# Kernel tuning notes

Measured on AMD Instinct MI355X. Metric: run time of the kernel, lower is better.

The kernel has to match this reference:

```python
import jax, jax.numpy as jnp
import numpy as np

N = 8192      # num_nodes
D_IN = 561    # input feature dim (HAR)
D_H = 256     # hidden / encoder dim
E = 262144    # edges per view (~32 avg degree)
NCLS = 6
LAMBDA = 1.0


def _gat_att(row, col, H, v0, v1, n):
    # per-edge sigmoid logits + row-wise segment softmax (sparse_softmax)
    f1 = (H @ v0)[:, 0]                      # (N,)
    f2 = (H @ v1)[:, 0]
    u = jax.nn.sigmoid(f1[row] + f2[col])    # (E,)
    rmax = jax.ops.segment_max(u, row, num_segments=n)
    ex = jnp.exp(u - rmax[row])
    rsum = jax.ops.segment_sum(ex, row, num_segments=n)
    return ex / (rsum[row] + 1e-12)


def _spmm(row, col, vals, H, n):
    # sparse.mm(C, H): out[row] += vals * H[col]
    return jax.ops.segment_sum(vals[:, None] * H[col], row, num_segments=n)


def setup_inputs() -> dict:
    key = jax.random.key(0)
    ks = jax.random.split(key, 30)

    def xav(k, shp):
        lim = np.sqrt(6.0 / (shp[0] + shp[1]))
        return jax.random.uniform(k, shp, jnp.float32, -lim, lim)

    inp = {}
    inp["X"] = jax.random.normal(ks[0], (N, D_IN), jnp.float32)
    inp["X2"] = jax.random.normal(ks[1], (N, D_IN), jnp.float32)
    inp["Theta"] = jax.random.normal(ks[2], (N, N), jnp.float32)
    inp["A_idx"] = jax.random.randint(ks[3], (2, E), 0, N)
    inp["A_vals"] = jax.random.uniform(ks[4], (E,), jnp.float32)
    inp["A2_idx"] = jax.random.randint(ks[5], (2, E), 0, N)
    inp["A2_vals"] = jax.random.uniform(ks[6], (E,), jnp.float32)
    inp["S"] = jax.random.randint(ks[7], (E,), 0, N)
    inp["R"] = jax.random.randint(ks[8], (E,), 0, N)
    inp["S2"] = jax.random.randint(ks[9], (E,), 0, N)
    inp["R2"] = jax.random.randint(ks[10], (E,), 0, N)
    inp["p"] = jax.random.randint(ks[11], (N,), 0, NCLS)
    inp["Labels"] = jax.random.randint(ks[12], (N,), 0, NCLS)
    # parameters (single encoder layer, shared across views as in the source)
    inp["W0"] = xav(ks[13], (D_IN, D_H))
    inp["v00"] = xav(ks[14], (D_H, 1))
    inp["v10"] = xav(ks[15], (D_H, 1))
    inp["weight"] = jnp.full((N, N), 1e-4, jnp.float32)
    inp["fc1_w"] = xav(ks[16], (512, D_H))
    inp["fc1_b"] = jnp.zeros((512,), jnp.float32)
    inp["fcz_w"] = xav(ks[17], (NCLS, 512))
    inp["fcz_b"] = jnp.zeros((NCLS,), jnp.float32)
    inp["fc2_w"] = xav(ks[18], (512, D_H))
    inp["fc2_b"] = jnp.zeros((512,), jnp.float32)
    inp["fcz2_w"] = xav(ks[19], (NCLS, 512))
    inp["fcz2_b"] = jnp.zeros((NCLS,), jnp.float32)
    return inp


def reference(X, X2, Theta, A_idx, A_vals, A2_idx, A2_vals, S, R, S2, R2, p, Labels,
              W0, v00, v10, weight, fc1_w, fc1_b, fcz_w, fcz_b,
              fc2_w, fc2_b, fcz2_w, fcz2_b):
    n = weight.shape[0]
    coef = weight - jnp.diag(jnp.diagonal(weight))   # zero the diagonal
    rowA, colA = A_idx[0], A_idx[1]
    rowB, colB = A2_idx[0], A2_idx[1]

    # ---- view 1: encode -> self-expression -> decode ----
    H = X @ W0                                        # (N, D_H)
    att1 = _gat_att(rowA, colA, H, v00, v10, n)       # (E,)
    H_enc1 = _spmm(rowA, colA, att1, H, n)            # (N, D_H)
    HC = coef @ H_enc1                                # (N, D_H)
    X_recon = _spmm(rowA, colA, att1, HC @ W0.T, n)   # (N, D_IN)
    z = (H_enc1 @ fc1_w.T + fc1_b) @ fcz_w.T + fcz_b  # (N, 6)

    # ---- view 2 (shares W0/v00/v10 as in the source) ----
    H2 = X2 @ W0
    att2 = _gat_att(rowB, colB, H2, v00, v10, n)
    H_enc2 = _spmm(rowB, colB, att2, H2, n)
    HC2 = coef @ H_enc2
    X2_recon = _spmm(rowB, colB, att2, HC2 @ W0.T, n)
    z2 = (H_enc2 @ fc2_w.T + fc2_b) @ fcz2_w.T + fcz2_b

    # ---- losses ----
    features_loss = ((X - X_recon) ** 2).sum() + ((X2 - X2_recon) ** 2).sum()
    SE_loss = 0.5 * ((H_enc1 - HC) ** 2).sum() + 0.5 * ((H_enc2 - HC2) ** 2).sum()
    S_Regular = jnp.abs(coef).sum()
    Cq_loss = jnp.abs(coef.T * Theta).sum()

    def ce_sum(logits):
        lp = jax.nn.log_softmax(logits, axis=-1)
        return -jnp.take_along_axis(lp, p[:, None], axis=1).sum()

    dense_loss = ce_sum(z) + ce_sum(z2)

    structure_loss = (-jax.nn.log_sigmoid((H_enc1[S] * H_enc1[R]).sum(-1)).sum()
                      - jax.nn.log_sigmoid((H_enc2[S2] * H_enc2[R2]).sum(-1)).sum())
    consistent_loss = ((H_enc1 - H_enc2) ** 2).sum()

    pre_loss = (features_loss + LAMBDA * structure_loss + 10.0 * SE_loss
                + 0.01 * consistent_loss + 1.0 * S_Regular)
    loss = (0.01 * features_loss + LAMBDA * structure_loss + 10.0 * SE_loss
            + 0.001 * consistent_loss + 1.0 * S_Regular + 5.0 * Cq_loss
            + 5.0 * dense_loss)
    return (pre_loss, loss, dense_loss, features_loss, structure_loss, SE_loss,
            coef, consistent_loss, S_Regular, Cq_loss, H_enc1, H_enc2)
```

## Files before the change

kernel.cpp:

```cpp
#include <hip/hip_runtime.h>
#include <math.h>

#define NNODES 8192
#define DIN 561
#define DH 256
#define NEDGE 262144
#define FCDIM 512
#define MLD 576

enum { AC_FEAT = 0, AC_STRUCT, AC_SE, AC_CONS, AC_SREG, AC_CQ, AC_DENSE, AC_NUM };
#define NBUCKET 64

#define OFF_COEF ((size_t)6)
#define OFF_CONS ((size_t)6 + (size_t)NNODES * NNODES)
#define OFF_SREG (OFF_CONS + 1)
#define OFF_CQ   (OFF_CONS + 2)
#define OFF_H1   (OFF_CONS + 3)
#define OFF_H2   (OFF_H1 + (size_t)NNODES * DH)

typedef short bf16x8 __attribute__((ext_vector_type(8)));
typedef float f32x4  __attribute__((ext_vector_type(4)));

__device__ __forceinline__ unsigned short f2bf(float f) {
    union { float f; unsigned int u; } v; v.f = f;
    const unsigned int u = v.u;
    return (unsigned short)((u + 0x7fffu + ((u >> 16) & 1u)) >> 16);
}

__device__ __forceinline__ void gload_lds16(const void* g, void* l) {
    __builtin_amdgcn_global_load_lds(
        (const __attribute__((address_space(1))) unsigned int*)g,
        (__attribute__((address_space(3))) unsigned int*)l, 16, 0, 0);
}

__global__ __launch_bounds__(256) void gate_gemm_nn(
    const float* __restrict__ A, const float* __restrict__ B,
    float* __restrict__ C, int M, int Nn, int K, int lda, int ldb, int ldc)
{
    __shared__ float As[32][68];
    __shared__ float Bs[32][68];
    const int bm = blockIdx.x * 64, bn = blockIdx.y * 64;
    const int tid = threadIdx.x;
    const int tx = tid & 15, ty = tid >> 4;
    float acc[4][4] = {};
    for (int k0 = 0; k0 < K; k0 += 32) {
        const int ar = tid >> 2, ak = (tid & 3) * 8;
        #pragma unroll
        for (int j = 0; j < 8; ++j) {
            const int gk = k0 + ak + j;
            As[ak + j][ar] = (gk < K) ? A[(size_t)(bm + ar) * lda + gk] : 0.f;
        }
        const int bk = tid >> 3, bn0 = (tid & 7) * 8;
        const int gk = k0 + bk;
        #pragma unroll
        for (int j = 0; j < 8; ++j) {
            const int gn = bn + bn0 + j;
            Bs[bk][bn0 + j] = (gk < K && gn < Nn) ? B[(size_t)gk * ldb + gn] : 0.f;
        }
        __syncthreads();
        #pragma unroll
        for (int k = 0; k < 32; ++k) {
            float a[4], b[4];
            #pragma unroll
            for (int i = 0; i < 4; ++i) a[i] = As[k][ty * 4 + i];
            #pragma unroll
            for (int j = 0; j < 4; ++j) b[j] = Bs[k][tx * 4 + j];
            #pragma unroll
            for (int i = 0; i < 4; ++i)
                #pragma unroll
                for (int j = 0; j < 4; ++j) acc[i][j] = fmaf(a[i], b[j], acc[i][j]);
        }
        __syncthreads();
    }
    #pragma unroll
    for (int i = 0; i < 4; ++i) {
        const int gm = bm + ty * 4 + i;
        if (gm >= M) continue;
        #pragma unroll
        for (int j = 0; j < 4; ++j) {
            const int gn = bn + tx * 4 + j;
            if (gn < Nn) C[(size_t)gm * ldc + gn] = acc[i][j];
        }
    }
}

__global__ __launch_bounds__(256) void gate_gemm_bt(
    const float* __restrict__ A, int lda,
    const float* __restrict__ B,
    const float* __restrict__ bias,
    float* __restrict__ C, int ldc, int M, int Nn, int K)
{
    __shared__ float As[32][68];
    __shared__ float Bs[32][68];
    const int bm = blockIdx.x * 64, bn = blockIdx.y * 64;
    const int tid = threadIdx.x;
    const int tx = tid & 15, ty = tid >> 4;
    float acc[4][4] = {};
    for (int k0 = 0; k0 < K; k0 += 32) {
        const int ar = tid >> 2, ak = (tid & 3) * 8;
        #pragma unroll
        for (int j = 0; j < 8; ++j)
            As[ak + j][ar] = A[(size_t)(bm + ar) * lda + k0 + ak + j];
        const int br = tid >> 2, bk = (tid & 3) * 8;
        const int gn = bn + br;
        #pragma unroll
        for (int j = 0; j < 8; ++j)
            Bs[bk + j][br] = (gn < Nn) ? B[(size_t)gn * K + k0 + bk + j] : 0.f;
        __syncthreads();
        #pragma unroll
        for (int k = 0; k < 32; ++k) {
            float a[4], b[4];
            #pragma unroll
            for (int i = 0; i < 4; ++i) a[i] = As[k][ty * 4 + i];
            #pragma unroll
            for (int j = 0; j < 4; ++j) b[j] = Bs[k][tx * 4 + j];
            #pragma unroll
            for (int i = 0; i < 4; ++i)
                #pragma unroll
                for (int j = 0; j < 4; ++j) acc[i][j] = fmaf(a[i], b[j], acc[i][j]);
        }
        __syncthreads();
    }
    #pragma unroll
    for (int i = 0; i < 4; ++i) {
        const int gm = bm + ty * 4 + i;
        if (gm >= M) continue;
        #pragma unroll
        for (int j = 0; j < 4; ++j) {
            const int gn = bn + tx * 4 + j;
            if (gn < Nn) {
                float v = acc[i][j];
                if (bias) v += bias[gn];
                C[(size_t)gm * ldc + gn] = v;
            }
        }
    }
}

__global__ __launch_bounds__(256) void gate_gemm_coef(
    const float* __restrict__ W, const float* __restrict__ B, float* __restrict__ C)
{
    __shared__ float As[16][132];
    __shared__ float Bs[16][64];
    const int bm = blockIdx.x * 128, bn = blockIdx.y * 64;
    const int tid = threadIdx.x;
    const int tx = tid & 15, ty = tid >> 4;
    float acc[8][4] = {};
    for (int k0 = 0; k0 < NNODES; k0 += 16) {
        const int ar = tid >> 1, ak = (tid & 1) * 8;
        const float* Ap = W + (size_t)(bm + ar) * NNODES + k0 + ak;
        const bool maskdiag = (k0 + 15 >= bm) && (k0 <= bm + 127);
        if (maskdiag) {
            #pragma unroll
            for (int j = 0; j < 8; ++j) {
                float v = Ap[j];
                if (bm + ar == k0 + ak + j) v = 0.f;
                As[ak + j][ar] = v;
            }
        } else {
            const float4 v0 = *(const float4*)(Ap);
            const float4 v1 = *(const float4*)(Ap + 4);
            As[ak + 0][ar] = v0.x; As[ak + 1][ar] = v0.y;
            As[ak + 2][ar] = v0.z; As[ak + 3][ar] = v0.w;
            As[ak + 4][ar] = v1.x; As[ak + 5][ar] = v1.y;
            As[ak + 6][ar] = v1.z; As[ak + 7][ar] = v1.w;
        }
        const int bk = tid >> 4, bn0 = (tid & 15) * 4;
        *(float4*)&Bs[bk][bn0] = *(const float4*)(B + (size_t)(k0 + bk) * 512 + bn + bn0);
        __syncthreads();
        #pragma unroll
        for (int k = 0; k < 16; ++k) {
            float a[8], b[4];
            #pragma unroll
            for (int i = 0; i < 8; ++i) a[i] = As[k][ty * 8 + i];
            #pragma unroll
            for (int j = 0; j < 4; ++j) b[j] = Bs[k][tx * 4 + j];
            #pragma unroll
            for (int i = 0; i < 8; ++i)
                #pragma unroll
                for (int j = 0; j < 4; ++j) acc[i][j] = fmaf(a[i], b[j], acc[i][j]);
        }
        __syncthreads();
    }
    #pragma unroll
    for (int i = 0; i < 8; ++i) {
        float4 v = make_float4(acc[i][0], acc[i][1], acc[i][2], acc[i][3]);
        *(float4*)(C + (size_t)(bm + ty * 8 + i) * 512 + bn + tx * 4) = v;
    }
}

#define BMT 128
#define BNT 64
#define BKT 64

__global__ __launch_bounds__(256, 2) void gate_gemm_coef_mfma(
    const unsigned short* __restrict__ Wbf,
    const unsigned short* __restrict__ Bt,
    float* __restrict__ C)
{
    __shared__ __align__(16) unsigned short Asm[2][BMT * BKT];
    __shared__ __align__(16) unsigned short Bsm[2][BNT * BKT];
    const int tid = threadIdx.x;
    const int wid = tid >> 6, lane = tid & 63;
    const int bm = blockIdx.x * BMT, bn = blockIdx.y * BNT;
    const int wr = wid >> 1, wc = wid & 1;

    const int l3 = lane >> 3, l7 = lane & 7;
    const int kxor = (l7 ^ l3) * 8;
    const unsigned short* aSrc[4];
    int aDst[4];
    #pragma unroll
    for (int i = 0; i < 4; ++i) {
        const int c = wid + i * 4;
        const int r = c * 8 + l3;
        aSrc[i] = Wbf + (size_t)(bm + r) * NNODES + kxor;
        aDst[i] = c * 512;
    }
    const unsigned short* bSrc[2];
    int bDst[2];
    #pragma unroll
    for (int i = 0; i < 2; ++i) {
        const int c = wid + i * 4;
        const int r = c * 8 + l3;
        bSrc[i] = Bt + (size_t)(bn + r) * NNODES + kxor;
        bDst[i] = c * 512;
    }

    const int l15 = lane & 15, l4 = lane >> 4;
    int aOff[2][4], bOff[2][2];
    #pragma unroll
    for (int ks = 0; ks < 2; ++ks) {
        const int u = ks * 4 + l4;
        #pragma unroll
        for (int mr = 0; mr < 4; ++mr) {
            const int r = wr * 64 + mr * 16 + l15;
            aOff[ks][mr] = r * 64 + ((u ^ (r & 7)) * 8);
        }
        #pragma unroll
        for (int nr = 0; nr < 2; ++nr) {
            const int r = wc * 32 + nr * 16 + l15;
            bOff[ks][nr] = r * 64 + ((u ^ (r & 7)) * 8);
        }
    }

    f32x4 acc[4][2];
    #pragma unroll
    for (int i = 0; i < 4; ++i)
        #pragma unroll
        for (int j = 0; j < 2; ++j) acc[i][j] = (f32x4){0.f, 0.f, 0.f, 0.f};

    #pragma unroll
    for (int i = 0; i < 4; ++i) { gload_lds16(aSrc[i], &Asm[0][aDst[i]]); aSrc[i] += BKT; }
    #pragma unroll
    for (int i = 0; i < 2; ++i) { gload_lds16(bSrc[i], &Bsm[0][bDst[i]]); bSrc[i] += BKT; }
    __syncthreads();

    int cur = 0;
    const int NT = NNODES / BKT;
    for (int t = 0; t < NT; ++t) {
        if (t + 1 < NT) {
            const int nxt = cur ^ 1;
            #pragma unroll
            for (int i = 0; i < 4; ++i) { gload_lds16(aSrc[i], &Asm[nxt][aDst[i]]); aSrc[i] += BKT; }
            #pragma unroll
            for (int i = 0; i < 2; ++i) { gload_lds16(bSrc[i], &Bsm[nxt][bDst[i]]); bSrc[i] += BKT; }
        }
        const unsigned short* Ab = &Asm[cur][0];
        const unsigned short* Bb = &Bsm[cur][0];
        #pragma unroll
        for (int ks = 0; ks < 2; ++ks) {
            bf16x8 av[4], bv[2];
            #pragma unroll
            for (int mr = 0; mr < 4; ++mr) av[mr] = *(const bf16x8*)(Ab + aOff[ks][mr]);
            #pragma unroll
            for (int nr = 0; nr < 2; ++nr) bv[nr] = *(const bf16x8*)(Bb + bOff[ks][nr]);
            #pragma unroll
            for (int mr = 0; mr < 4; ++mr)
                #pragma unroll
                for (int nr = 0; nr < 2; ++nr)
                    acc[mr][nr] = __builtin_amdgcn_mfma_f32_16x16x32_bf16(
                        av[mr], bv[nr], acc[mr][nr], 0, 0, 0);
        }
        __syncthreads();
        cur ^= 1;
    }

    #pragma unroll
    for (int mr = 0; mr < 4; ++mr) {
        const int grow0 = bm + wr * 64 + mr * 16 + l4 * 4;
        #pragma unroll
        for (int nr = 0; nr < 2; ++nr) {
            const int gcol = bn + wc * 32 + nr * 16 + l15;
            float* cp = C + (size_t)grow0 * 512 + gcol;
            #pragma unroll
            for (int q = 0; q < 4; ++q) cp[(size_t)q * 512] = acc[mr][nr][q];
        }
    }
}

__global__ __launch_bounds__(256) void gate_hcat_bt(
    const float* __restrict__ Hcat, unsigned short* __restrict__ Bt)
{
    __shared__ float Ts[64][65];
    const int i0 = blockIdx.x * 64;
    const int j0 = blockIdx.y * 64;
    const int c = threadIdx.x & 63, g = threadIdx.x >> 6;
    #pragma unroll
    for (int ii = 0; ii < 16; ++ii) {
        const int r = g * 16 + ii;
        Ts[r][c] = Hcat[(size_t)(i0 + r) * 512 + j0 + c];
    }
    __syncthreads();
    #pragma unroll
    for (int ii = 0; ii < 16; ++ii) {
        const int r = g * 16 + ii;
        Bt[(size_t)(j0 + r) * NNODES + i0 + c] = f2bf(Ts[c][r]);
    }
}

__global__ __launch_bounds__(256) void gate_f1f2(
    const float* __restrict__ H, const float* __restrict__ v0,
    const float* __restrict__ v1, float* __restrict__ f1, float* __restrict__ f2)
{
    const int wave = threadIdx.x >> 6, lane = threadIdx.x & 63;
    const int row = blockIdx.x * 4 + wave;
    const float4 h = ((const float4*)(H + (size_t)row * DH))[lane];
    const float4 a = ((const float4*)v0)[lane];
    const float4 b = ((const float4*)v1)[lane];
    float s1 = h.x * a.x + h.y * a.y + h.z * a.z + h.w * a.w;
    float s2 = h.x * b.x + h.y * b.y + h.z * b.z + h.w * b.w;
    #pragma unroll
    for (int off = 32; off; off >>= 1) {
        s1 += __shfl_down(s1, off);
        s2 += __shfl_down(s2, off);
    }
    if (lane == 0) { f1[row] = s1; f2[row] = s2; }
}

__global__ void gate_hist(const int* __restrict__ rows, int* __restrict__ cnt)
{
    const int e = blockIdx.x * 256 + threadIdx.x;
    if (e < NEDGE) atomicAdd(&cnt[rows[e]], 1);
}

__global__ __launch_bounds__(256) void gate_scan(
    const int* __restrict__ cnt, int* __restrict__ rowptr, int* __restrict__ cur)
{
    __shared__ int part[256];
    const int t = threadIdx.x;
    const int base = t * 32;
    int local[32];
    int s = 0;
    #pragma unroll
    for (int i = 0; i < 32; ++i) { local[i] = s; s += cnt[base + i]; }
    part[t] = s;
    __syncthreads();
    for (int d = 1; d < 256; d <<= 1) {
        const int add = (t >= d) ? part[t - d] : 0;
        __syncthreads();
        part[t] += add;
        __syncthreads();
    }
    const int excl = (t == 0) ? 0 : part[t - 1];
    #pragma unroll
    for (int i = 0; i < 32; ++i) {
        const int v = excl + local[i];
        rowptr[base + i] = v;
        cur[base + i] = v;
    }
    if (t == 255) rowptr[NNODES] = excl + s;
}

__global__ void gate_scatter(const int* __restrict__ rows, const int* __restrict__ cols,
                             int* __restrict__ cur, int* __restrict__ col_p)
{
    const int e = blockIdx.x * 256 + threadIdx.x;
    if (e < NEDGE) {
        const int slot = atomicAdd(&cur[rows[e]], 1);
        col_p[slot] = cols[e];
    }
}

__global__ __launch_bounds__(64) void gate_att(
    const int* __restrict__ rowptr, const int* __restrict__ col_p,
    const float* __restrict__ f1, const float* __restrict__ f2,
    float* __restrict__ att_p)
{
    const int row = blockIdx.x;
    const int s0 = rowptr[row], s1 = rowptr[row + 1];
    const int lane = threadIdx.x;
    const float f1r = f1[row];
    float mx = -1e30f;
    for (int s = s0 + lane; s < s1; s += 64) {
        float u = f1r + f2[col_p[s]];
        u = 1.f / (1.f + expf(-u));
        att_p[s] = u;
        mx = fmaxf(mx, u);
    }
    #pragma unroll
    for (int off = 32; off; off >>= 1) mx = fmaxf(mx, __shfl_xor(mx, off));
    float sum = 0.f;
    for (int s = s0 + lane; s < s1; s += 64) {
        const float ex = expf(att_p[s] - mx);
        att_p[s] = ex;
        sum += ex;
    }
    #pragma unroll
    for (int off = 32; off; off >>= 1) sum += __shfl_xor(sum, off);
    const float inv = 1.f / (sum + 1e-12f);
    for (int s = s0 + lane; s < s1; s += 64) att_p[s] *= inv;
}

__global__ __launch_bounds__(256) void gate_spmm_henc(
    const int* __restrict__ rowptr, const int* __restrict__ col_p,
    const float* __restrict__ att_p, const float* __restrict__ H,
    float* __restrict__ Hcat, float* __restrict__ outp, int voff)
{
    const int row = blockIdx.x, d = threadIdx.x;
    const int s0 = rowptr[row], s1 = rowptr[row + 1];
    float acc = 0.f;
    for (int s = s0; s < s1; ++s)
        acc = fmaf(att_p[s], H[(size_t)col_p[s] * DH + d], acc);
    Hcat[(size_t)row * 512 + voff + d] = acc;
    outp[(size_t)row * DH + d] = acc;
}

__global__ __launch_bounds__(256) void gate_coef(
    const float* __restrict__ W, const float* __restrict__ Theta,
    float* __restrict__ coef_out, double* __restrict__ accumB,
    unsigned short* __restrict__ wbf)
{
    __shared__ float Ts[64][65];
    __shared__ float red[256];
    const int i0 = blockIdx.x * 64, j0 = blockIdx.y * 64;
    const int t = threadIdx.x;
    const int c = t & 63, rgrp = t >> 6;
    #pragma unroll
    for (int jj = 0; jj < 16; ++jj) {
        const int jr = rgrp * 16 + jj;
        Ts[jr][c] = Theta[(size_t)(j0 + jr) * NNODES + i0 + c];
    }
    __syncthreads();
    float sreg = 0.f, cq = 0.f;
    #pragma unroll
    for (int ii = 0; ii < 16; ++ii) {
        const int rr = rgrp * 16 + ii;
        const int gi = i0 + rr, gj = j0 + c;
        const float w = W[(size_t)gi * NNODES + gj];
        const float cf = (gi == gj) ? 0.f : w;
        coef_out[(size_t)gi * NNODES + gj] = cf;
        if (wbf) wbf[(size_t)gi * NNODES + gj] = f2bf(cf);
        const float a = fabsf(cf);
        sreg += a;
        cq = fmaf(a, fabsf(Ts[c][rr]), cq);
    }
    const int bucket = (blockIdx.x + blockIdx.y) & (NBUCKET - 1);
    red[t] = sreg; __syncthreads();
    for (int d = 128; d; d >>= 1) { if (t < d) red[t] += red[t + d]; __syncthreads(); }
    if (t == 0) atomicAdd(&accumB[bucket * AC_NUM + AC_SREG], (double)red[0]);
    __syncthreads();
    red[t] = cq; __syncthreads();
    for (int d = 128; d; d >>= 1) { if (t < d) red[t] += red[t + d]; __syncthreads(); }
    if (t == 0) atomicAdd(&accumB[bucket * AC_NUM + AC_CQ], (double)red[0]);
}

__global__ __launch_bounds__(256) void gate_se(
    const float* __restrict__ Hcat, const float* __restrict__ HC,
    double* __restrict__ accumB)
{
    __shared__ float red[256];
    float part = 0.f;
    for (size_t i = (size_t)blockIdx.x * 256 + threadIdx.x;
         i < (size_t)NNODES * 512; i += (size_t)2048 * 256) {
        const float d = Hcat[i] - HC[i];
        part = fmaf(d, d, part);
    }
    const int t = threadIdx.x;
    red[t] = part; __syncthreads();
    for (int d = 128; d; d >>= 1) { if (t < d) red[t] += red[t + d]; __syncthreads(); }
    if (t == 0) atomicAdd(&accumB[(blockIdx.x & (NBUCKET - 1)) * AC_NUM + AC_SE], (double)red[0]);
}

__global__ __launch_bounds__(256) void gate_cons(
    const float* __restrict__ Hcat, double* __restrict__ accumB)
{
    __shared__ float red[256];
    float part = 0.f;
    for (size_t i = (size_t)blockIdx.x * 256 + threadIdx.x;
         i < (size_t)NNODES * DH; i += (size_t)1024 * 256) {
        const size_t row = i >> 8;
        const int d = (int)(i & 255);
        const float v = Hcat[row * 512 + d] - Hcat[row * 512 + 256 + d];
        part = fmaf(v, v, part);
    }
    const int t = threadIdx.x;
    red[t] = part; __syncthreads();
    for (int d = 128; d; d >>= 1) { if (t < d) red[t] += red[t + d]; __syncthreads(); }
    if (t == 0) atomicAdd(&accumB[(blockIdx.x & (NBUCKET - 1)) * AC_NUM + AC_CONS], (double)red[0]);
}

__global__ __launch_bounds__(256) void gate_recon_loss(
    const int* __restrict__ rowptr, const int* __restrict__ col_p,
    const float* __restrict__ att_p, const float* __restrict__ Mbuf,
    const float* __restrict__ X, double* __restrict__ accumB)
{
    __shared__ float red[256];
    const int row = blockIdx.x, t = threadIdx.x;
    const int s0 = rowptr[row], s1 = rowptr[row + 1];
    float acc0 = 0.f, acc1 = 0.f, acc2 = 0.f;
    for (int s = s0; s < s1; ++s) {
        const float a = att_p[s];
        const float* mr = Mbuf + (size_t)col_p[s] * MLD;
        acc0 = fmaf(a, mr[t], acc0);
        acc1 = fmaf(a, mr[t + 256], acc1);
        if (t < DIN - 512) acc2 = fmaf(a, mr[t + 512], acc2);
    }
    const float* xr = X + (size_t)row * DIN;
    const float d0 = xr[t] - acc0;
    const float d1 = xr[t + 256] - acc1;
    float part = d0 * d0 + d1 * d1;
    if (t < DIN - 512) { const float d2 = xr[t + 512] - acc2; part = fmaf(d2, d2, part); }
    red[t] = part; __syncthreads();
    for (int d = 128; d; d >>= 1) { if (t < d) red[t] += red[t + d]; __syncthreads(); }
    if (t == 0) atomicAdd(&accumB[(blockIdx.x & (NBUCKET - 1)) * AC_NUM + AC_FEAT], (double)red[0]);
}

__global__ __launch_bounds__(256) void gate_struct(
    const int* __restrict__ S, const int* __restrict__ R,
    const float* __restrict__ Hcat, int voff, double* __restrict__ accumB)
{
    __shared__ float red[4];
    const int wave = threadIdx.x >> 6, lane = threadIdx.x & 63;
    const int widx = blockIdx.x * 4 + wave;
    float part = 0.f;
    for (int e = widx; e < NEDGE; e += gridDim.x * 4) {
        const float4 av = ((const float4*)(Hcat + (size_t)S[e] * 512 + voff))[lane];
        const float4 bv = ((const float4*)(Hcat + (size_t)R[e] * 512 + voff))[lane];
        float d = av.x * bv.x + av.y * bv.y + av.z * bv.z + av.w * bv.w;
        #pragma unroll
        for (int off = 32; off; off >>= 1) d += __shfl_xor(d, off);
        if (lane == 0) {
            const float x = d;
            const float sp = (x > 0.f) ? log1pf(expf(-x)) : (-x + log1pf(expf(x)));
            part += sp;
        }
    }
    if (lane == 0) red[wave] = part;
    __syncthreads();
    if (threadIdx.x == 0)
        atomicAdd(&accumB[(blockIdx.x & (NBUCKET - 1)) * AC_NUM + AC_STRUCT],
                  (double)(red[0] + red[1] + red[2] + red[3]));
}

__global__ __launch_bounds__(256) void gate_zhead(
    const float* __restrict__ tbuf, const float* __restrict__ fczw,
    const float* __restrict__ fczb, const int* __restrict__ p,
    double* __restrict__ accumB)
{
    __shared__ float wz[6 * 512];
    __shared__ float bz[6];
    __shared__ float red[4];
    for (int i = threadIdx.x; i < 6 * 512; i += 256) wz[i] = fczw[i];
    if (threadIdx.x < 6) bz[threadIdx.x] = fczb[threadIdx.x];
    __syncthreads();
    const int wave = threadIdx.x >> 6, lane = threadIdx.x & 63;
    const int row = blockIdx.x * 4 + wave;
    const float* tr = tbuf + (size_t)row * 512;
    float part[6] = {};
    for (int j = lane; j < 512; j += 64) {
        const float tv = tr[j];
        #pragma unroll
        for (int c = 0; c < 6; ++c) part[c] = fmaf(tv, wz[c * 512 + j], part[c]);
    }
    #pragma unroll
    for (int c = 0; c < 6; ++c)
        #pragma unroll
        for (int off = 32; off; off >>= 1) part[c] += __shfl_xor(part[c], off);
    if (lane == 0) {
        float z[6], mx = -1e30f;
        #pragma unroll
        for (int c = 0; c < 6; ++c) { z[c] = part[c] + bz[c]; mx = fmaxf(mx, z[c]); }
        float se = 0.f;
        #pragma unroll
        for (int c = 0; c < 6; ++c) se += expf(z[c] - mx);
        const float lse = mx + logf(se);
        red[wave] = lse - z[p[row]];
    }
    __syncthreads();
    if (threadIdx.x == 0)
        atomicAdd(&accumB[(blockIdx.x & (NBUCKET - 1)) * AC_NUM + AC_DENSE],
                  (double)(red[0] + red[1] + red[2] + red[3]));
}

__global__ void gate_final(const double* __restrict__ accumB, float* __restrict__ out)
{
    if (threadIdx.x == 0 && blockIdx.x == 0) {
        double acc[AC_NUM];
        for (int i = 0; i < AC_NUM; ++i) acc[i] = 0.0;
        for (int b = 0; b < NBUCKET; ++b)
            for (int i = 0; i < AC_NUM; ++i) acc[i] += accumB[b * AC_NUM + i];
        const double feat = acc[AC_FEAT], st = acc[AC_STRUCT];
        const double se = 0.5 * acc[AC_SE];
        const double cons = acc[AC_CONS], sreg = acc[AC_SREG];
        const double cq = acc[AC_CQ], dl = acc[AC_DENSE];
        const double pre = feat + st + 10.0 * se + 0.01 * cons + sreg;
        const double loss = 0.01 * feat + st + 10.0 * se + 0.001 * cons + sreg
                          + 5.0 * cq + 5.0 * dl;
        out[0] = (float)pre;
        out[1] = (float)loss;
        out[2] = (float)dl;
        out[3] = (float)feat;
        out[4] = (float)st;
        out[5] = (float)se;
        out[OFF_CONS] = (float)cons;
        out[OFF_SREG] = (float)sreg;
        out[OFF_CQ]   = (float)cq;
    }
}

extern "C" void kernel_launch(void* const* d_in, const int* in_sizes, int n_in,
                              void* d_out, int out_size, void* d_ws, size_t ws_size,
                              hipStream_t stream)
{
    (void)in_sizes; (void)n_in; (void)out_size;
    const float* X      = (const float*)d_in[0];
    const float* X2     = (const float*)d_in[1];
    const float* Theta  = (const float*)d_in[2];
    const int*   Aidx   = (const int*)d_in[3];
    const int*   A2idx  = (const int*)d_in[5];
    const int*   S      = (const int*)d_in[7];
    const int*   R      = (const int*)d_in[8];
    const int*   S2     = (const int*)d_in[9];
    const int*   R2     = (const int*)d_in[10];
    const int*   p      = (const int*)d_in[11];
    const float* W0     = (const float*)d_in[13];
    const float* v00    = (const float*)d_in[14];
    const float* v10    = (const float*)d_in[15];
    const float* weight = (const float*)d_in[16];
    const float* fc1_w  = (const float*)d_in[17];
    const float* fc1_b  = (const float*)d_in[18];
    const float* fcz_w  = (const float*)d_in[19];
    const float* fcz_b  = (const float*)d_in[20];
    const float* fc2_w  = (const float*)d_in[21];
    const float* fc2_b  = (const float*)d_in[22];
    const float* fcz2_w = (const float*)d_in[23];
    const float* fcz2_b = (const float*)d_in[24];
    float* out = (float*)d_out;

    char* wp = (char*)d_ws;
    auto alloc = [&](size_t bytes) -> void* {
        void* r = (void*)wp;
        wp += (bytes + 255) & ~(size_t)255;
        return r;
    };
    float* H1    = (float*)alloc((size_t)NNODES * DH * 4);
    float* H2    = (float*)alloc((size_t)NNODES * DH * 4);
    float* Hcat  = (float*)alloc((size_t)NNODES * 512 * 4);
    float* HCcat = (float*)alloc((size_t)NNODES * 512 * 4);
    float* Mbuf  = (float*)alloc((size_t)NNODES * MLD * 4);
    float* tbuf  = Mbuf;
    float* f1a = (float*)alloc(NNODES * 4);
    float* f2a = (float*)alloc(NNODES * 4);
    float* f1b = (float*)alloc(NNODES * 4);
    float* f2b = (float*)alloc(NNODES * 4);
    int* cnt    = (int*)alloc(2 * NNODES * 4);
    int* rowptr = (int*)alloc(2 * (NNODES + 1) * 4);
    int* cur    = (int*)alloc(2 * NNODES * 4);
    int* colp   = (int*)alloc(2 * (size_t)NEDGE * 4);
    float* attp = (float*)alloc(2 * (size_t)NEDGE * 4);
    double* accumB = (double*)alloc(NBUCKET * AC_NUM * 8);
    unsigned short* Wbf = (unsigned short*)alloc((size_t)NNODES * NNODES * 2);
    unsigned short* Bt  = (unsigned short*)alloc((size_t)512 * NNODES * 2);
    const bool use_mfma = ((size_t)(wp - (char*)d_ws) <= ws_size);

    hipMemsetAsync(cnt, 0, 2 * NNODES * 4, stream);
    hipMemsetAsync(accumB, 0, NBUCKET * AC_NUM * 8, stream);

    gate_gemm_nn<<<dim3(NNODES / 64, DH / 64), 256, 0, stream>>>(
        X, W0, H1, NNODES, DH, DIN, DIN, DH, DH);
    gate_gemm_nn<<<dim3(NNODES / 64, DH / 64), 256, 0, stream>>>(
        X2, W0, H2, NNODES, DH, DIN, DIN, DH, DH);
    gate_f1f2<<<NNODES / 4, 256, 0, stream>>>(H1, v00, v10, f1a, f2a);
    gate_f1f2<<<NNODES / 4, 256, 0, stream>>>(H2, v00, v10, f1b, f2b);

    gate_hist<<<NEDGE / 256, 256, 0, stream>>>(Aidx, cnt);
    gate_hist<<<NEDGE / 256, 256, 0, stream>>>(A2idx, cnt + NNODES);
    gate_scan<<<1, 256, 0, stream>>>(cnt, rowptr, cur);
    gate_scan<<<1, 256, 0, stream>>>(cnt + NNODES, rowptr + NNODES + 1, cur + NNODES);
    gate_scatter<<<NEDGE / 256, 256, 0, stream>>>(Aidx, Aidx + NEDGE, cur, colp);
    gate_scatter<<<NEDGE / 256, 256, 0, stream>>>(A2idx, A2idx + NEDGE, cur + NNODES, colp + NEDGE);

    gate_att<<<NNODES, 64, 0, stream>>>(rowptr, colp, f1a, f2a, attp);
    gate_att<<<NNODES, 64, 0, stream>>>(rowptr + NNODES + 1, colp + NEDGE, f1b, f2b, attp + NEDGE);
    gate_spmm_henc<<<NNODES, 256, 0, stream>>>(rowptr, colp, attp, H1, Hcat, out + OFF_H1, 0);
    gate_spmm_henc<<<NNODES, 256, 0, stream>>>(rowptr + NNODES + 1, colp + NEDGE, attp + NEDGE,
                                               H2, Hcat, out + OFF_H2, 256);

    gate_coef<<<dim3(NNODES / 64, NNODES / 64), 256, 0, stream>>>(
        weight, Theta, out + OFF_COEF, accumB, use_mfma ? Wbf : nullptr);

    if (use_mfma) {
        gate_hcat_bt<<<dim3(NNODES / 64, 512 / 64), 256, 0, stream>>>(Hcat, Bt);
        gate_gemm_coef_mfma<<<dim3(NNODES / BMT, 512 / BNT), 256, 0, stream>>>(Wbf, Bt, HCcat);
    } else {
        gate_gemm_coef<<<dim3(NNODES / 128, 512 / 64), 256, 0, stream>>>(weight, Hcat, HCcat);
    }

    gate_se<<<2048, 256, 0, stream>>>(Hcat, HCcat, accumB);
    gate_cons<<<1024, 256, 0, stream>>>(Hcat, accumB);

    gate_gemm_bt<<<dim3(NNODES / 64, (DIN + 63) / 64), 256, 0, stream>>>(
        HCcat, 512, W0, nullptr, Mbuf, MLD, NNODES, DIN, DH);
    gate_recon_loss<<<NNODES, 256, 0, stream>>>(rowptr, colp, attp, Mbuf, X, accumB);
    gate_gemm_bt<<<dim3(NNODES / 64, (DIN + 63) / 64), 256, 0, stream>>>(
        HCcat + 256, 512, W0, nullptr, Mbuf, MLD, NNODES, DIN, DH);
    gate_recon_loss<<<NNODES, 256, 0, stream>>>(rowptr + NNODES + 1, colp + NEDGE,
                                                attp + NEDGE, Mbuf, X2, accumB);

    gate_gemm_bt<<<dim3(NNODES / 64, FCDIM / 64), 256, 0, stream>>>(
        Hcat, 512, fc1_w, fc1_b, tbuf, 512, NNODES, FCDIM, DH);
    gate_zhead<<<NNODES / 4, 256, 0, stream>>>(tbuf, fcz_w, fcz_b, p, accumB);
    gate_gemm_bt<<<dim3(NNODES / 64, FCDIM / 64), 256, 0, stream>>>(
        Hcat + 256, 512, fc2_w, fc2_b, tbuf, 512, NNODES, FCDIM, DH);
    gate_zhead<<<NNODES / 4, 256, 0, stream>>>(tbuf, fcz2_w, fcz2_b, p, accumB);

    gate_struct<<<2048, 256, 0, stream>>>(S, R, Hcat, 0, accumB);
    gate_struct<<<2048, 256, 0, stream>>>(S2, R2, Hcat, 256, accumB);

    gate_final<<<1, 64, 0, stream>>>(accumB, out);
}
```

Baseline: 1.819 ms.

## Reassociate reconstruction and fold linear z-heads to cut GEMM and gather cost

The reconstruction now aggregates HC over the sparse attention first, at width 256 instead of 561, converts the result to bf16 and runs an MFMA GEMM against W0 with the squared-error loss fused into the epilogue. The two-layer linear z-head (fc1 then fcz) is collapsed into one 6x256 weight plus bias, which removes the NxN512 intermediate GEMMs. The structure loss reads a bf16 copy of Hcat, which halves the gather bytes. In exchange it adds bf16 rounding in the recon GEMM and the structure dot products, which could shift the loss values, and a small per-call weight-folding kernel.

```diff
diff --git a/kernel.cpp b/kernel.cpp
--- a/kernel.cpp
+++ b/kernel.cpp
@@ -5,8 +5,6 @@
 #define DIN 561
 #define DH 256
 #define NEDGE 262144
-#define FCDIM 512
-#define MLD 576
 
 enum { AC_FEAT = 0, AC_STRUCT, AC_SE, AC_CONS, AC_SREG, AC_CQ, AC_DENSE, AC_NUM };
 #define NBUCKET 64
@@ -25,6 +23,10 @@
     union { float f; unsigned int u; } v; v.f = f;
     const unsigned int u = v.u;
     return (unsigned short)((u + 0x7fffu + ((u >> 16) & 1u)) >> 16);
+}
+__device__ __forceinline__ float bf2f(unsigned short u) {
+    union { unsigned int u; float f; } v; v.u = ((unsigned int)u) << 16;
+    return v.f;
 }
 
 __device__ __forceinline__ void gload_lds16(const void* g, void* l) {
@@ -80,59 +82,6 @@
         for (int j = 0; j < 4; ++j) {
             const int gn = bn + tx * 4 + j;
             if (gn < Nn) C[(size_t)gm * ldc + gn] = acc[i][j];
-        }
-    }
-}
-
-__global__ __launch_bounds__(256) void gate_gemm_bt(
-    const float* __restrict__ A, int lda,
-    const float* __restrict__ B,
-    const float* __restrict__ bias,
-    float* __restrict__ C, int ldc, int M, int Nn, int K)
-{
-    __shared__ float As[32][68];
-    __shared__ float Bs[32][68];
-    const int bm = blockIdx.x * 64, bn = blockIdx.y * 64;
-    const int tid = threadIdx.x;
-    const int tx = tid & 15, ty = tid >> 4;
-    float acc[4][4] = {};
-    for (int k0 = 0; k0 < K; k0 += 32) {
-        const int ar = tid >> 2, ak = (tid & 3) * 8;
-        #pragma unroll
-        for (int j = 0; j < 8; ++j)
-            As[ak + j][ar] = A[(size_t)(bm + ar) * lda + k0 + ak + j];
-        const int br = tid >> 2, bk = (tid & 3) * 8;
-        const int gn = bn + br;
-        #pragma unroll
-        for (int j = 0; j < 8; ++j)
-            Bs[bk + j][br] = (gn < Nn) ? B[(size_t)gn * K + k0 + bk + j] : 0.f;
-        __syncthreads();
-        #pragma unroll
-        for (int k = 0; k < 32; ++k) {
-            float a[4], b[4];
-            #pragma unroll
-            for (int i = 0; i < 4; ++i) a[i] = As[k][ty * 4 + i];
-            #pragma unroll
-            for (int j = 0; j < 4; ++j) b[j] = Bs[k][tx * 4 + j];
-            #pragma unroll
-            for (int i = 0; i < 4; ++i)
-                #pragma unroll
-                for (int j = 0; j < 4; ++j) acc[i][j] = fmaf(a[i], b[j], acc[i][j]);
-        }
-        __syncthreads();
-    }
-    #pragma unroll
-    for (int i = 0; i < 4; ++i) {
-        const int gm = bm + ty * 4 + i;
-        if (gm >= M) continue;
-        #pragma unroll
-        for (int j = 0; j < 4; ++j) {
-            const int gn = bn + tx * 4 + j;
-            if (gn < Nn) {
-                float v = acc[i][j];
-                if (bias) v += bias[gn];
-                C[(size_t)gm * ldc + gn] = v;
-            }
         }
     }
 }
@@ -298,6 +247,124 @@
     }
 }
 
+__global__ __launch_bounds__(256, 2) void gate_mfma_recon(
+    const unsigned short* __restrict__ Abf,
+    const unsigned short* __restrict__ Bbf,
+    const float* __restrict__ X,
+    double* __restrict__ accumB)
+{
+    __shared__ __align__(16) unsigned short Asm[2][BMT * BKT];
+    __shared__ __align__(16) unsigned short Bsm[2][BNT * BKT];
+    __shared__ float red[256];
+    const int tid = threadIdx.x;
+    const int wid = tid >> 6, lane = tid & 63;
+    const int bm = blockIdx.x * BMT, bn = blockIdx.y * BNT;
+    const int wr = wid >> 1, wc = wid & 1;
+
+    const int l3 = lane >> 3, l7 = lane & 7;
+    const int kxor = (l7 ^ l3) * 8;
+    const unsigned short* aSrc[4];
+    int aDst[4];
+    #pragma unroll
+    for (int i = 0; i < 4; ++i) {
+        const int c = wid + i * 4;
+        const int r = c * 8 + l3;
+        aSrc[i] = Abf + (size_t)(bm + r) * DH + kxor;
+        aDst[i] = c * 512;
+    }
+    const unsigned short* bSrc[2];
+    int bDst[2];
+    #pragma unroll
+    for (int i = 0; i < 2; ++i) {
+        const int c = wid + i * 4;
+        const int r = c * 8 + l3;
+        bSrc[i] = Bbf + (size_t)(bn + r) * DH + kxor;
+        bDst[i] = c * 512;
+    }
+
+    const int l15 = lane & 15, l4 = lane >> 4;
+    int aOff[2][4], bOff[2][2];
+    #pragma unroll
+    for (int ks = 0; ks < 2; ++ks) {
+        const int u = ks * 4 + l4;
+        #pragma unroll
+        for (int mr = 0; mr < 4; ++mr) {
+            const int r = wr * 64 + mr * 16 + l15;
+            aOff[ks][mr] = r * 64 + ((u ^ (r & 7)) * 8);
+        }
+        #pragma unroll
+        for (int nr = 0; nr < 2; ++nr) {
+            const int r = wc * 32 + nr * 16 + l15;
+            bOff[ks][nr] = r * 64 + ((u ^ (r & 7)) * 8);
+        }
+    }
+
+    f32x4 acc[4][2];
+    #pragma unroll
+    for (int i = 0; i < 4; ++i)
+        #pragma unroll
+        for (int j = 0; j < 2; ++j) acc[i][j] = (f32x4){0.f, 0.f, 0.f, 0.f};
+
+    #pragma unroll
+    for (int i = 0; i < 4; ++i) { gload_lds16(aSrc[i], &Asm[0][aDst[i]]); aSrc[i] += BKT; }
+    #pragma unroll
+    for (int i = 0; i < 2; ++i) { gload_lds16(bSrc[i], &Bsm[0][bDst[i]]); bSrc[i] += BKT; }
+    __syncthreads();
+
+    int cur = 0;
+    const int NT = DH / BKT;
+    for (int t = 0; t < NT; ++t) {
+        if (t + 1 < NT) {
+            const int nxt = cur ^ 1;
+            #pragma unroll
+            for (int i = 0; i < 4; ++i) { gload_lds16(aSrc[i], &Asm[nxt][aDst[i]]); aSrc[i] += BKT; }
+            #pragma unroll
+            for (int i = 0; i < 2; ++i) { gload_lds16(bSrc[i], &Bsm[nxt][bDst[i]]); bSrc[i] += BKT; }
+        }
+        const unsigned short* Ab = &Asm[cur][0];
+        const unsigned short* Bb = &Bsm[cur][0];
+        #pragma unroll
+        for (int ks = 0; ks < 2; ++ks) {
+            bf16x8 av[4], bv[2];
+            #pragma unroll
+            for (int mr = 0; mr < 4; ++mr) av[mr] = *(const bf16x8*)(Ab + aOff[ks][mr]);
+            #pragma unroll
+            for (int nr = 0; nr < 2; ++nr) bv[nr] = *(const bf16x8*)(Bb + bOff[ks][nr]);
+            #pragma unroll
+            for (int mr = 0; mr < 4; ++mr)
+                #pragma unroll
+                for (int nr = 0; nr < 2; ++nr)
+                    acc[mr][nr] = __builtin_amdgcn_mfma_f32_16x16x32_bf16(
+                        av[mr], bv[nr], acc[mr][nr], 0, 0, 0);
+        }
+        __syncthreads();
+        cur ^= 1;
+    }
+
+    float part = 0.f;
+    #pragma unroll
+    for (int mr = 0; mr < 4; ++mr) {
+        const int grow0 = bm + wr * 64 + mr * 16 + l4 * 4;
+        #pragma unroll
+        for (int nr = 0; nr < 2; ++nr) {
+            const int gcol = bn + wc * 32 + nr * 16 + l15;
+            if (gcol < DIN) {
+                const float* xp = X + (size_t)grow0 * DIN + gcol;
+                #pragma unroll
+                for (int q = 0; q < 4; ++q) {
+                    const float d = xp[(size_t)q * DIN] - acc[mr][nr][q];
+                    part = fmaf(d, d, part);
+                }
+            }
+        }
+    }
+    red[tid] = part; __syncthreads();
+    for (int d = 128; d; d >>= 1) { if (tid < d) red[tid] += red[tid + d]; __syncthreads(); }
+    if (tid == 0)
+        atomicAdd(&accumB[((blockIdx.x + blockIdx.y) & (NBUCKET - 1)) * AC_NUM + AC_FEAT],
+                  (double)red[0]);
+}
+
 __global__ __launch_bounds__(256) void gate_hcat_bt(
     const float* __restrict__ Hcat, unsigned short* __restrict__ Bt)
 {
@@ -316,6 +383,87 @@
         const int r = g * 16 + ii;
         Bt[(size_t)(j0 + r) * NNODES + i0 + c] = f2bf(Ts[c][r]);
     }
+}
+
+__global__ __launch_bounds__(256) void gate_w0bf(
+    const float* __restrict__ W0, unsigned short* __restrict__ w0bf)
+{
+    const int idx = blockIdx.x * 256 + threadIdx.x;
+    const int n = idx >> 8;
+    w0bf[idx] = (n < DIN) ? f2bf(W0[idx]) : (unsigned short)0;
+}
+
+__global__ __launch_bounds__(256) void gate_zfold(
+    const float* __restrict__ fc1w_1, const float* __restrict__ fc1b_1,
+    const float* __restrict__ fczw_1, const float* __restrict__ fczb_1,
+    const float* __restrict__ fc1w_2, const float* __restrict__ fc1b_2,
+    const float* __restrict__ fczw_2, const float* __restrict__ fczb_2,
+    float* __restrict__ zw1, float* __restrict__ zw2)
+{
+    const float* fc1w = blockIdx.x ? fc1w_2 : fc1w_1;
+    const float* fc1b = blockIdx.x ? fc1b_2 : fc1b_1;
+    const float* fczw = blockIdx.x ? fczw_2 : fczw_1;
+    const float* fczb = blockIdx.x ? fczb_2 : fczb_1;
+    float* zw = blockIdx.x ? zw2 : zw1;
+    __shared__ float wcz[6 * 512];
+    __shared__ float b1s[512];
+    const int t = threadIdx.x;
+    for (int i = t; i < 6 * 512; i += 256) wcz[i] = fczw[i];
+    for (int i = t; i < 512; i += 256) b1s[i] = fc1b[i];
+    __syncthreads();
+    float acc[6] = {};
+    for (int j = 0; j < 512; ++j) {
+        const float w = fc1w[(size_t)j * DH + t];
+        #pragma unroll
+        for (int c = 0; c < 6; ++c) acc[c] = fmaf(wcz[c * 512 + j], w, acc[c]);
+    }
+    #pragma unroll
+    for (int c = 0; c < 6; ++c) zw[c * DH + t] = acc[c];
+    if (t < 6) {
+        float s = fczb[t];
+        for (int j = 0; j < 512; ++j) s = fmaf(wcz[t * 512 + j], b1s[j], s);
+        zw[6 * DH + t] = s;
+    }
+}
+
+__global__ __launch_bounds__(256) void gate_zhead2(
+    const float* __restrict__ Hcat, int voff, const float* __restrict__ zwb,
+    const int* __restrict__ p, double* __restrict__ accumB)
+{
+    __shared__ float zw[6 * DH];
+    __shared__ float zb[6];
+    __shared__ float red[4];
+    const int t = threadIdx.x;
+    for (int i = t; i < 6 * DH; i += 256) zw[i] = zwb[i];
+    if (t < 6) zb[t] = zwb[6 * DH + t];
+    __syncthreads();
+    const int wave = t >> 6, lane = t & 63;
+    const int row = blockIdx.x * 4 + wave;
+    const float4 h = ((const float4*)(Hcat + (size_t)row * 512 + voff))[lane];
+    float part[6];
+    #pragma unroll
+    for (int c = 0; c < 6; ++c) {
+        const float4 w = *(const float4*)&zw[c * DH + lane * 4];
+        part[c] = h.x * w.x + h.y * w.y + h.z * w.z + h.w * w.w;
+    }
+    #pragma unroll
+    for (int c = 0; c < 6; ++c)
+        #pragma unroll
+        for (int off = 32; off; off >>= 1) part[c] += __shfl_xor(part[c], off);
+    if (lane == 0) {
+        float z[6], mx = -1e30f;
+        #pragma unroll
+        for (int c = 0; c < 6; ++c) { z[c] = part[c] + zb[c]; mx = fmaxf(mx, z[c]); }
+        float se = 0.f;
+        #pragma unroll
+        for (int c = 0; c < 6; ++c) se += expf(z[c] - mx);
+        const float lse = mx + logf(se);
+        red[wave] = lse - z[p[row]];
+    }
+    __syncthreads();
+    if (t == 0)
+        atomicAdd(&accumB[(blockIdx.x & (NBUCKET - 1)) * AC_NUM + AC_DENSE],
+                  (double)(red[0] + red[1] + red[2] + red[3]));
 }
 
 __global__ __launch_bounds__(256) void gate_f1f2(
@@ -414,7 +562,8 @@
 __global__ __launch_bounds__(256) void gate_spmm_henc(
     const int* __restrict__ rowptr, const int* __restrict__ col_p,
     const float* __restrict__ att_p, const float* __restrict__ H,
-    float* __restrict__ Hcat, float* __restrict__ outp, int voff)
+    float* __restrict__ Hcat, unsigned short* __restrict__ Hcatbf,
+    float* __restrict__ outp, int voff)
 {
     const int row = blockIdx.x, d = threadIdx.x;
     const int s0 = rowptr[row], s1 = rowptr[row + 1];
@@ -422,7 +571,21 @@
     for (int s = s0; s < s1; ++s)
         acc = fmaf(att_p[s], H[(size_t)col_p[s] * DH + d], acc);
     Hcat[(size_t)row * 512 + voff + d] = acc;
+    Hcatbf[(size_t)row * 512 + voff + d] = f2bf(acc);
     outp[(size_t)row * DH + d] = acc;
+}
+
+__global__ __launch_bounds__(256) void gate_spmm_phc(
+    const int* __restrict__ rowptr, const int* __restrict__ col_p,
+    const float* __restrict__ att_p, const float* __restrict__ HCcat,
+    int voff, unsigned short* __restrict__ PHCbf)
+{
+    const int row = blockIdx.x, d = threadIdx.x;
+    const int s0 = rowptr[row], s1 = rowptr[row + 1];
+    float acc = 0.f;
+    for (int s = s0; s < s1; ++s)
+        acc = fmaf(att_p[s], HCcat[(size_t)col_p[s] * 512 + voff + d], acc);
+    PHCbf[(size_t)row * DH + d] = f2bf(acc);
 }
 
 __global__ __launch_bounds__(256) void gate_coef(
@@ -499,44 +662,19 @@
     if (t == 0) atomicAdd(&accumB[(blockIdx.x & (NBUCKET - 1)) * AC_NUM + AC_CONS], (double)red[0]);
 }
 
-__global__ __launch_bounds__(256) void gate_recon_loss(
-    const int* __restrict__ rowptr, const int* __restrict__ col_p,
-    const float* __restrict__ att_p, const float* __restrict__ Mbuf,
-    const float* __restrict__ X, double* __restrict__ accumB)
-{
-    __shared__ float red[256];
-    const int row = blockIdx.x, t = threadIdx.x;
-    const int s0 = rowptr[row], s1 = rowptr[row + 1];
-    float acc0 = 0.f, acc1 = 0.f, acc2 = 0.f;
-    for (int s = s0; s < s1; ++s) {
-        const float a = att_p[s];
-        const float* mr = Mbuf + (size_t)col_p[s] * MLD;
-        acc0 = fmaf(a, mr[t], acc0);
-        acc1 = fmaf(a, mr[t + 256], acc1);
-        if (t < DIN - 512) acc2 = fmaf(a, mr[t + 512], acc2);
-    }
-    const float* xr = X + (size_t)row * DIN;
-    const float d0 = xr[t] - acc0;
-    const float d1 = xr[t + 256] - acc1;
-    float part = d0 * d0 + d1 * d1;
-    if (t < DIN - 512) { const float d2 = xr[t + 512] - acc2; part = fmaf(d2, d2, part); }
-    red[t] = part; __syncthreads();
-    for (int d = 128; d; d >>= 1) { if (t < d) red[t] += red[t + d]; __syncthreads(); }
-    if (t == 0) atomicAdd(&accumB[(blockIdx.x & (NBUCKET - 1)) * AC_NUM + AC_FEAT], (double)red[0]);
-}
-
 __global__ __launch_bounds__(256) void gate_struct(
     const int* __restrict__ S, const int* __restrict__ R,
-    const float* __restrict__ Hcat, int voff, double* __restrict__ accumB)
+    const unsigned short* __restrict__ Hcatbf, int voff, double* __restrict__ accumB)
 {
     __shared__ float red[4];
     const int wave = threadIdx.x >> 6, lane = threadIdx.x & 63;
     const int widx = blockIdx.x * 4 + wave;
     float part = 0.f;
     for (int e = widx; e < NEDGE; e += gridDim.x * 4) {
-        const float4 av = ((const float4*)(Hcat + (size_t)S[e] * 512 + voff))[lane];
-        const float4 bv = ((const float4*)(Hcat + (size_t)R[e] * 512 + voff))[lane];
-        float d = av.x * bv.x + av.y * bv.y + av.z * bv.z + av.w * bv.w;
+        const ushort4 av = ((const ushort4*)(Hcatbf + (size_t)S[e] * 512 + voff))[lane];
+        const ushort4 bv = ((const ushort4*)(Hcatbf + (size_t)R[e] * 512 + voff))[lane];
+        float d = bf2f(av.x) * bf2f(bv.x) + bf2f(av.y) * bf2f(bv.y)
+                + bf2f(av.z) * bf2f(bv.z) + bf2f(av.w) * bf2f(bv.w);
         #pragma unroll
         for (int off = 32; off; off >>= 1) d += __shfl_xor(d, off);
         if (lane == 0) {
@@ -549,46 +687,6 @@
     __syncthreads();
     if (threadIdx.x == 0)
         atomicAdd(&accumB[(blockIdx.x & (NBUCKET - 1)) * AC_NUM + AC_STRUCT],
-                  (double)(red[0] + red[1] + red[2] + red[3]));
-}
-
-__global__ __launch_bounds__(256) void gate_zhead(
-    const float* __restrict__ tbuf, const float* __restrict__ fczw,
-    const float* __restrict__ fczb, const int* __restrict__ p,
-    double* __restrict__ accumB)
-{
-    __shared__ float wz[6 * 512];
-    __shared__ float bz[6];
-    __shared__ float red[4];
-    for (int i = threadIdx.x; i < 6 * 512; i += 256) wz[i] = fczw[i];
-    if (threadIdx.x < 6) bz[threadIdx.x] = fczb[threadIdx.x];
-    __syncthreads();
-    const int wave = threadIdx.x >> 6, lane = threadIdx.x & 63;
-    const int row = blockIdx.x * 4 + wave;
-    const float* tr = tbuf + (size_t)row * 512;
-    float part[6] = {};
-    for (int j = lane; j < 512; j += 64) {
-        const float tv = tr[j];
-        #pragma unroll
-        for (int c = 0; c < 6; ++c) part[c] = fmaf(tv, wz[c * 512 + j], part[c]);
-    }
-    #pragma unroll
-    for (int c = 0; c < 6; ++c)
-        #pragma unroll
-        for (int off = 32; off; off >>= 1) part[c] += __shfl_xor(part[c], off);
-    if (lane == 0) {
-        float z[6], mx = -1e30f;
-        #pragma unroll
-        for (int c = 0; c < 6; ++c) { z[c] = part[c] + bz[c]; mx = fmaxf(mx, z[c]); }
-        float se = 0.f;
-        #pragma unroll
-        for (int c = 0; c < 6; ++c) se += expf(z[c] - mx);
-        const float lse = mx + logf(se);
-        red[wave] = lse - z[p[row]];
-    }
-    __syncthreads();
-    if (threadIdx.x == 0)
-        atomicAdd(&accumB[(blockIdx.x & (NBUCKET - 1)) * AC_NUM + AC_DENSE],
                   (double)(red[0] + red[1] + red[2] + red[3]));
 }
 
@@ -657,8 +755,11 @@
     float* H2    = (float*)alloc((size_t)NNODES * DH * 4);
     float* Hcat  = (float*)alloc((size_t)NNODES * 512 * 4);
     float* HCcat = (float*)alloc((size_t)NNODES * 512 * 4);
-    float* Mbuf  = (float*)alloc((size_t)NNODES * MLD * 4);
-    float* tbuf  = Mbuf;
+    unsigned short* Hcatbf = (unsigned short*)alloc((size_t)NNODES * 512 * 2);
+    unsigned short* PHCbf  = (unsigned short*)alloc((size_t)NNODES * DH * 2);
+    unsigned short* w0bf   = (unsigned short*)alloc((size_t)576 * DH * 2);
+    float* zw1 = (float*)alloc((6 * DH + 8) * 4);
+    float* zw2 = (float*)alloc((6 * DH + 8) * 4);
     float* f1a = (float*)alloc(NNODES * 4);
     float* f2a = (float*)alloc(NNODES * 4);
     float* f1b = (float*)alloc(NNODES * 4);
@@ -676,6 +777,10 @@
     hipMemsetAsync(cnt, 0, 2 * NNODES * 4, stream);
     hipMemsetAsync(accumB, 0, NBUCKET * AC_NUM * 8, stream);
 
+    gate_w0bf<<<576, 256, 0, stream>>>(W0, w0bf);
+    gate_zfold<<<2, 256, 0, stream>>>(fc1_w, fc1_b, fcz_w, fcz_b,
+                                      fc2_w, fc2_b, fcz2_w, fcz2_b, zw1, zw2);
+
     gate_gemm_nn<<<dim3(NNODES / 64, DH / 64), 256, 0, stream>>>(
         X, W0, H1, NNODES, DH, DIN, DIN, DH, DH);
     gate_gemm_nn<<<dim3(NNODES / 64, DH / 64), 256, 0, stream>>>(
@@ -692,9 +797,10 @@
 
     gate_att<<<NNODES, 64, 0, stream>>>(rowptr, colp, f1a, f2a, attp);
     gate_att<<<NNODES, 64, 0, stream>>>(rowptr + NNODES + 1, colp + NEDGE, f1b, f2b, attp + NEDGE);
-    gate_spmm_henc<<<NNODES, 256, 0, stream>>>(rowptr, colp, attp, H1, Hcat, out + OFF_H1, 0);
+    gate_spmm_henc<<<NNODES, 256, 0, stream>>>(rowptr, colp, attp, H1, Hcat, Hcatbf,
+                                               out + OFF_H1, 0);
     gate_spmm_henc<<<NNODES, 256, 0, stream>>>(rowptr + NNODES + 1, colp + NEDGE, attp + NEDGE,
-                                               H2, Hcat, out + OFF_H2, 256);
+                                               H2, Hcat, Hcatbf, out + OFF_H2, 256);
 
     gate_coef<<<dim3(NNODES / 64, NNODES / 64), 256, 0, stream>>>(
         weight, Theta, out + OFF_COEF, accumB, use_mfma ? Wbf : nullptr);
@@ -709,23 +815,17 @@
     gate_se<<<2048, 256, 0, stream>>>(Hcat, HCcat, accumB);
     gate_cons<<<1024, 256, 0, stream>>>(Hcat, accumB);
 
-    gate_gemm_bt<<<dim3(NNODES / 64, (DIN + 63) / 64), 256, 0, stream>>>(
-        HCcat, 512, W0, nullptr, Mbuf, MLD, NNODES, DIN, DH);
-    gate_recon_loss<<<NNODES, 256, 0, stream>>>(rowptr, colp, attp, Mbuf, X, accumB);
-    gate_gemm_bt<<<dim3(NNODES / 64, (DIN + 63) / 64), 256, 0, stream>>>(
-        HCcat + 256, 512, W0, nullptr, Mbuf, MLD, NNODES, DIN, DH);
-    gate_recon_loss<<<NNODES, 256, 0, stream>>>(rowptr + NNODES + 1, colp + NEDGE,
-                                                attp + NEDGE, Mbuf, X2, accumB);
-
-    gate_gemm_bt<<<dim3(NNODES / 64, FCDIM / 64), 256, 0, stream>>>(
-        Hcat, 512, fc1_w, fc1_b, tbuf, 512, NNODES, FCDIM, DH);
-    gate_zhead<<<NNODES / 4, 256, 0, stream>>>(tbuf, fcz_w, fcz_b, p, accumB);
-    gate_gemm_bt<<<dim3(NNODES / 64, FCDIM / 64), 256, 0, stream>>>(
-        Hcat + 256, 512, fc2_w, fc2_b, tbuf, 512, NNODES, FCDIM, DH);
-    gate_zhead<<<NNODES / 4, 256, 0, stream>>>(tbuf, fcz2_w, fcz2_b, p, accumB);
-
-    gate_struct<<<2048, 256, 0, stream>>>(S, R, Hcat, 0, accumB);
-    gate_struct<<<2048, 256, 0, stream>>>(S2, R2, Hcat, 256, accumB);
+    gate_spmm_phc<<<NNODES, 256, 0, stream>>>(rowptr, colp, attp, HCcat, 0, PHCbf);
+    gate_mfma_recon<<<dim3(NNODES / BMT, 576 / BNT), 256, 0, stream>>>(PHCbf, w0bf, X, accumB);
+    gate_spmm_phc<<<NNODES, 256, 0, stream>>>(rowptr + NNODES + 1, colp + NEDGE, attp + NEDGE,
+                                              HCcat, 256, PHCbf);
+    gate_mfma_recon<<<dim3(NNODES / BMT, 576 / BNT), 256, 0, stream>>>(PHCbf, w0bf, X2, accumB);
+
+    gate_zhead2<<<NNODES / 4, 256, 0, stream>>>(Hcat, 0, zw1, p, accumB);
+    gate_zhead2<<<NNODES / 4, 256, 0, stream>>>(Hcat, 256, zw2, p, accumB);
+
+    gate_struct<<<2048, 256, 0, stream>>>(S, R, Hcatbf, 0, accumB);
+    gate_struct<<<2048, 256, 0, stream>>>(S2, R2, Hcatbf, 256, accumB);
 
     gate_final<<<1, 64, 0, stream>>>(accumB, out);
 }
```

Result: faster. 1.678 ms (-7.7%).
